# Kernel optimization log

Measured on AMD Instinct MI355X. Metric: run time of the kernel, lower is better.

The kernel has to match this reference:

```python
import jax, jax.numpy as jnp
import numpy as np

B, N = 4, 512
H, NH, L = 64, 4, 3
HD = H // NH          # 16
NODE_F, EDGE_F = 18, 7
H4 = H // 4           # 16
FF = 4 * H            # 256


def _ln(x, g, b, eps=1e-5):
    m = jnp.mean(x, axis=-1, keepdims=True)
    v = jnp.mean((x - m) ** 2, axis=-1, keepdims=True)
    return (x - m) * jax.lax.rsqrt(v + eps) * g + b


def _leaky(x):
    return jnp.where(x >= 0, x, 0.2 * x)


def _spd(edge_mask):
    # Vectorized Floyd-Warshall, mirrors GraphTransformer._compute_spd_matrix
    n = edge_mask.shape[1]
    spd = jnp.where(edge_mask, 1.0, float(n)).astype(jnp.float32)
    i = jnp.arange(n)
    spd = spd.at[:, i, i].set(0.0)
    def body(k, s):
        col = jax.lax.dynamic_slice_in_dim(s, k, 1, axis=2)  # [B,N,1]
        row = jax.lax.dynamic_slice_in_dim(s, k, 1, axis=1)  # [B,1,N]
        return jnp.minimum(s, col + row)
    return jax.lax.fori_loop(0, n, body, spd)


def setup_inputs() -> dict:
    key = jax.random.key(0)
    ks = iter(jax.random.split(key, 64))
    def nrm(shape, s):
        return jax.random.normal(next(ks), shape, jnp.float32) * s
    inp = {}
    inp["node_features"] = jax.random.normal(next(ks), (B, N, NODE_F), jnp.float32)
    inp["edge_features"] = jax.random.normal(next(ks), (B, N, N, EDGE_F), jnp.float32)
    nm = jax.random.uniform(next(ks), (B, N)) < 0.9
    inp["node_mask"] = nm.at[:, 0].set(True)
    inp["edge_mask"] = jax.random.uniform(next(ks), (B, N, N)) < 0.05
    s_h = 1.0 / np.sqrt(H)
    inp["node_proj_w"] = nrm((NODE_F, H), 0.2)
    inp["node_proj_b"] = jnp.zeros((H,), jnp.float32)
    inp["edge_proj_w"] = nrm((EDGE_F, H), 0.2)
    inp["edge_proj_b"] = jnp.zeros((H,), jnp.float32)
    inp["wq"] = nrm((L, H, H), s_h)
    inp["wk"] = nrm((L, H, H), s_h)
    inp["wv"] = nrm((L, H, H), s_h)
    inp["eb1_w"] = nrm((L, H, H4), s_h)
    inp["eb1_b"] = jnp.zeros((L, H4), jnp.float32)
    inp["eb_ln_g"] = jnp.ones((L, H4), jnp.float32)
    inp["eb_ln_b"] = jnp.zeros((L, H4), jnp.float32)
    inp["eb2_w"] = nrm((L, H4, NH), 0.2)
    inp["eb2_b"] = jnp.zeros((L, NH), jnp.float32)
    inp["spd1_w"] = nrm((L, 1, H4), 0.5)
    inp["spd1_b"] = jnp.zeros((L, H4), jnp.float32)
    inp["spd2_w"] = nrm((L, H4, NH), 0.2)
    inp["spd2_b"] = jnp.zeros((L, NH), jnp.float32)
    inp["wo_w"] = nrm((L, H, H), s_h)
    inp["wo_b"] = jnp.zeros((L, H), jnp.float32)
    inp["ln1_g"] = jnp.ones((L, H), jnp.float32)
    inp["ln1_b"] = jnp.zeros((L, H), jnp.float32)
    inp["ln2_g"] = jnp.ones((L, H), jnp.float32)
    inp["ln2_b"] = jnp.zeros((L, H), jnp.float32)
    inp["ffn1_w"] = nrm((L, H, FF), s_h)
    inp["ffn1_b"] = jnp.zeros((L, FF), jnp.float32)
    inp["ffn2_w"] = nrm((L, FF, H), 1.0 / np.sqrt(FF))
    inp["ffn2_b"] = jnp.zeros((L, H), jnp.float32)
    inp["score1_w"] = nrm((2 * H, H), 1.0 / np.sqrt(2 * H))
    inp["score1_b"] = jnp.zeros((H,), jnp.float32)
    inp["score_ln_g"] = jnp.ones((H,), jnp.float32)
    inp["score_ln_b"] = jnp.zeros((H,), jnp.float32)
    inp["score2_w"] = nrm((H, 1), 0.1)
    inp["score2_b"] = jnp.zeros((1,), jnp.float32)
    return inp


def reference(node_features, edge_features, node_mask, edge_mask,
              node_proj_w, node_proj_b, edge_proj_w, edge_proj_b,
              wq, wk, wv,
              eb1_w, eb1_b, eb_ln_g, eb_ln_b, eb2_w, eb2_b,
              spd1_w, spd1_b, spd2_w, spd2_b,
              wo_w, wo_b, ln1_g, ln1_b, ln2_g, ln2_b,
              ffn1_w, ffn1_b, ffn2_w, ffn2_b,
              score1_w, score1_b, score_ln_g, score_ln_b, score2_w, score2_b):
    NEG = -1000000000.0
    h = node_features @ node_proj_w + node_proj_b            # [B,N,H]
    e = edge_features @ edge_proj_w + edge_proj_b            # [B,N,N,H]
    spd = _spd(edge_mask)
    spd_n = (jnp.clip(spd, 0.0, 10.0) / 10.0)[..., None]      # [B,N,N,1]
    scale = 1.0 / np.sqrt(HD)
    for l in range(L):
        Q = (h @ wq[l]).reshape(B, N, NH, HD)
        K = (h @ wk[l]).reshape(B, N, NH, HD)
        V = (h @ wv[l]).reshape(B, N, NH, HD)
        scores = jnp.einsum('bihd,bjhd->bhij', Q, K) * scale  # [B,NH,N,N]
        x = _leaky(_ln(e @ eb1_w[l] + eb1_b[l], eb_ln_g[l], eb_ln_b[l]))
        edge_bias = jnp.transpose(x @ eb2_w[l] + eb2_b[l], (0, 3, 1, 2))
        sb = _leaky(spd_n @ spd1_w[l] + spd1_b[l]) @ spd2_w[l] + spd2_b[l]
        spd_bias = jnp.transpose(sb, (0, 3, 1, 2))
        bias = jnp.where(edge_mask[:, None, :, :], edge_bias, spd_bias)
        scores = jnp.where(node_mask[:, None, None, :], scores + bias, NEG)
        attn = jax.nn.softmax(scores, axis=-1)
        out = jnp.einsum('bhij,bjhd->bihd', attn, V).reshape(B, N, H)
        out = out @ wo_w[l] + wo_b[l]
        h = _ln(h + out, ln1_g[l], ln1_b[l])
        ff = jax.nn.gelu(h @ ffn1_w[l] + ffn1_b[l], approximate=False) @ ffn2_w[l] + ffn2_b[l]
        h = _ln(h + ff, ln2_g[l], ln2_b[l])
    h_ego = jnp.broadcast_to(h[:, :1, :], (B, N - 1, H))
    hc = jnp.concatenate([h_ego, h[:, 1:, :]], axis=-1)       # [B,N-1,2H]
    x = _leaky(_ln(hc @ score1_w + score1_b, score_ln_g, score_ln_b))
    logits = (x @ score2_w + score2_b)[..., 0]                # [B,N-1]
    cand_mask = node_mask[:, 1:]
    no_cand = ~jnp.any(cand_mask, axis=-1)
    cand_mask = cand_mask.at[:, 0].set(cand_mask[:, 0] | no_cand)
    logits = jnp.where(cand_mask, logits, NEG)
    probs = jax.nn.softmax(logits, axis=-1)
    return probs, h
```

## Files before the change

kernel.cpp:

```cpp
#include <hip/hip_runtime.h>
#include <math.h>

typedef unsigned long long u64;
typedef unsigned int u32;

__device__ __forceinline__ float wsum(float x) {
#pragma unroll
    for (int o = 1; o < 64; o <<= 1) x += __shfl_xor(x, o);
    return x;
}
__device__ __forceinline__ float wmaxr(float x) {
#pragma unroll
    for (int o = 1; o < 64; o <<= 1) x = fmaxf(x, __shfl_xor(x, o));
    return x;
}

__global__ __launch_bounds__(256) void kA(
    const int* __restrict__ em, const float* __restrict__ nf,
    const float* __restrict__ npw, const float* __restrict__ npb,
    u64* __restrict__ adj, u32* __restrict__ elist, u32* __restrict__ rowCnt,
    float* __restrict__ hbuf)
{
    int t = threadIdx.x, wv = t >> 6, lane = t & 63;
    int g = blockIdx.x * 4 + wv;
    const int* emr = em + (size_t)g * 512;
    u32 run = 0;
#pragma unroll
    for (int s = 0; s < 8; ++s) {
        int j = s * 64 + lane;
        int v = emr[j];
        u64 bal = __ballot(v != 0);
        if (v != 0) {
            u32 slot = run + (u32)__popcll(bal & ((1ULL << lane) - 1ULL));
            if (slot < 96u) elist[g * 96 + slot] = (u32)j;
        }
        if (lane == 0) adj[(size_t)g * 8 + s] = bal;
        run += (u32)__popcll(bal);
    }
    if (lane == 0) rowCnt[g] = run < 96u ? run : 96u;
    float acc = npb[lane];
    const float* r = nf + (size_t)g * 18;
#pragma unroll
    for (int c = 0; c < 18; ++c) acc += r[c] * npw[c * 64 + lane];
    hbuf[(size_t)g * 64 + lane] = acc;
}

__global__ __launch_bounds__(256) void kB(
    const u64* __restrict__ adj, const float* __restrict__ ef,
    const u32* __restrict__ elist, const u32* __restrict__ rowCnt,
    const float* __restrict__ hbuf,
    const float* __restrict__ epw, const float* __restrict__ epb,
    const float* __restrict__ eb1w, const float* __restrict__ eb1b,
    const float* __restrict__ eblng, const float* __restrict__ eblnb,
    const float* __restrict__ eb2w, const float* __restrict__ eb2b,
    const float* __restrict__ wq, const float* __restrict__ wk, const float* __restrict__ wvw,
    unsigned char* __restrict__ spd, float* __restrict__ vals,
    float* __restrict__ Qb, float* __restrict__ KT, float* __restrict__ VT)
{
    __shared__ u64 adjL[4096];
    __shared__ u64 bfsS[4][24];
    __shared__ float MS[684];
    __shared__ u32 pool[384];
    __shared__ u32 offs[5];
    __shared__ u32 cA[4];
    __shared__ int votes[4];
    int t = threadIdx.x, wv = t >> 6, lane = t & 63;
    int g = blockIdx.x * 4 + wv;
    int b = g >> 9, srow = g & 511;
    {
        const float4* s = (const float4*)(adj + (size_t)b * 4096);
        float4* d = (float4*)adjL;
#pragma unroll
        for (int u = 0; u < 8; ++u) d[t + u * 256] = s[t + u * 256];
    }
    for (int u = t; u < 384; u += 256) {
        int l = u >> 7, r = u & 127, f = r >> 4, c = r & 15;
        const float* W1 = eb1w + l * 1024 + c;
        float s;
        if (f < 7) {
            s = 0.f;
            const float* ew = epw + f * 64;
            for (int k = 0; k < 64; ++k) s += ew[k] * W1[k * 16];
        } else {
            s = eb1b[l * 16 + c];
            for (int k = 0; k < 64; ++k) s += epb[k] * W1[k * 16];
        }
        MS[u] = s;
    }
    if (t < 192) MS[384 + t] = eb2w[t];
    if (t < 48) { MS[576 + t] = eblng[t]; MS[624 + t] = eblnb[t]; }
    if (t < 12) MS[672 + t] = eb2b[t];
    u64* vis = &bfsS[wv][0]; u64* fro = vis + 8; u64* nxt = vis + 16;
    if (lane < 8) {
        u64 iv = (lane == (srow >> 6)) ? (1ULL << (srow & 63)) : 0ULL;
        vis[lane] = iv; fro[lane] = iv; nxt[lane] = 0ULL;
    }
    __syncthreads();
    u64 myDist = 0x0A0A0A0A0A0A0A0AULL;
    if (lane == (srow >> 3)) myDist &= ~(0xFFULL << ((srow & 7) * 8));
    for (int d = 1; d <= 9; ++d) {
        int c = lane >> 3, w = lane & 7;
        u64 f = fro[c];
        u64 acc = 0ULL;
        while (f) {
            int k = (c << 6) + __builtin_ctzll(f);
            f &= f - 1;
            acc |= adjL[k * 8 + w];
        }
        if (acc) atomicOr(&nxt[w], acc);
        __syncthreads();
        u64 nw = 0ULL;
        if (lane < 8) {
            nw = nxt[lane] & ~vis[lane];
            vis[lane] |= nw; fro[lane] = nw; nxt[lane] = 0ULL;
        }
        u64 bal = __ballot(nw != 0ULL);
        if (lane == 0) votes[wv] = (bal != 0ULL) ? 1 : 0;
        __syncthreads();
        u64 fw = fro[lane >> 3];
        u32 bits = (u32)(fw >> ((lane & 7) * 8)) & 0xFFu;
        if (bits) {
            u64 bm = 0ULL;
#pragma unroll
            for (int kk = 0; kk < 8; ++kk) if (bits & (1u << kk)) bm |= 0xFFULL << (8 * kk);
            myDist = (myDist & ~bm) | ((0x0101010101010101ULL * (u64)(u32)d) & bm);
        }
        if (!(votes[0] | votes[1] | votes[2] | votes[3])) break;
    }
    ((u64*)spd)[(size_t)g * 64 + lane] = myDist;
    {
        float hv = hbuf[(size_t)g * 64 + lane];
        float aq = 0.f, ak = 0.f, av = 0.f;
        for (int k = 0; k < 64; ++k) {
            float hk = __shfl(hv, k);
            aq += hk * wq[k * 64 + lane];
            ak += hk * wk[k * 64 + lane];
            av += hk * wvw[k * 64 + lane];
        }
        Qb[(size_t)g * 64 + lane] = aq;
        KT[((size_t)(b * 64 + lane)) * 512 + srow] = ak;
        VT[((size_t)(b * 64 + lane)) * 512 + srow] = av;
    }
    u32 cnt = rowCnt[g];
    if (lane == 0) cA[wv] = cnt;
    __syncthreads();
    if (t == 0) {
        u32 a = 0;
        for (int i = 0; i < 4; ++i) { offs[i] = a; a += cA[i]; }
        offs[4] = a;
    }
    __syncthreads();
    u32 base = offs[wv];
    if (lane < (int)cnt)
        pool[base + lane] = ((u32)wv << 16) | ((u32)lane << 9) | elist[g * 96 + lane];
    if (lane + 64 < (int)cnt)
        pool[base + lane + 64] = ((u32)wv << 16) | ((u32)(lane + 64) << 9) | elist[g * 96 + lane + 64];
    __syncthreads();
    u32 tot = offs[4];
    for (u32 e = t; e < tot; e += 256) {
        u32 p = pool[e];
        int rl = (int)(p >> 16);
        u32 s = (p >> 9) & 127u;
        u32 j = p & 511u;
        int ge = blockIdx.x * 4 + rl;
        const float* e7 = ef + ((size_t)ge * 512 + j) * 7;
        float ff[7];
#pragma unroll
        for (int f = 0; f < 7; ++f) ff[f] = e7[f];
#pragma unroll 1
        for (int l = 0; l < 3; ++l) {
            float tt[16];
#pragma unroll
            for (int c = 0; c < 16; ++c) tt[c] = MS[(l * 8 + 7) * 16 + c];
#pragma unroll
            for (int f = 0; f < 7; ++f) {
                float fv = ff[f];
#pragma unroll
                for (int c = 0; c < 16; ++c) tt[c] += fv * MS[(l * 8 + f) * 16 + c];
            }
            float m = 0.f;
#pragma unroll
            for (int c = 0; c < 16; ++c) m += tt[c];
            m *= 0.0625f;
            float var = 0.f;
#pragma unroll
            for (int c = 0; c < 16; ++c) { float d = tt[c] - m; var += d * d; }
            var *= 0.0625f;
            float inv = rsqrtf(var + 1e-5f);
#pragma unroll
            for (int c = 0; c < 16; ++c) {
                float x = (tt[c] - m) * inv * MS[576 + l * 16 + c] + MS[624 + l * 16 + c];
                tt[c] = x >= 0.f ? x : 0.2f * x;
            }
#pragma unroll
            for (int hh = 0; hh < 4; ++hh) {
                float a = MS[672 + l * 4 + hh];
#pragma unroll
                for (int c = 0; c < 16; ++c) a += tt[c] * MS[384 + (l * 16 + c) * 4 + hh];
                vals[(u32)(l * 4 + hh) * 196608u + (u32)ge * 96u + s] = a;
            }
        }
    }
}

__global__ __launch_bounds__(256, 2) void kAttn(
    const float* __restrict__ Qb, const float* __restrict__ KTin, const float* __restrict__ VTin,
    const unsigned char* __restrict__ spd, const u32* __restrict__ elist,
    const u32* __restrict__ rowCnt, const float* __restrict__ vals,
    const float* __restrict__ s1w, const float* __restrict__ s1b,
    const float* __restrict__ s2w, const float* __restrict__ s2b,
    const int* __restrict__ nm, int l, float* __restrict__ attO)
{
    __shared__ float kt[8192];
    __shared__ float bv[8192];
    int t = threadIdx.x, wv = t >> 6, lane = t & 63;
    int bh = blockIdx.x >> 5;
    int tile = blockIdx.x & 31;
    int b = bh >> 2, hh = bh & 3;
    int i0 = tile * 16;
    int rbase = i0 + wv * 4;
    float qv = Qb[((size_t)(b * 512 + rbase + (lane >> 4))) * 64 + hh * 16 + (lane & 15)];
    float q[4][16];
#pragma unroll
    for (int r = 0; r < 4; ++r)
#pragma unroll
        for (int d = 0; d < 16; ++d) q[r][d] = __shfl(qv, r * 16 + d);
    {
        const float4* s = (const float4*)(KTin + ((size_t)(b * 64 + hh * 16)) * 512);
        float4* d = (float4*)kt;
#pragma unroll
        for (int u = 0; u < 8; ++u) d[t + u * 256] = s[t + u * 256];
    }
    float tval;
    {
        int li = lane < 11 ? lane : 10;
        float x = (float)li * 0.1f;
        float a = s2b[l * 4 + hh];
#pragma unroll
        for (int c = 0; c < 16; ++c) {
            float v = x * s1w[l * 16 + c] + s1b[l * 16 + c];
            v = v >= 0.f ? v : 0.2f * v;
            a += v * s2w[(l * 16 + c) * 4 + hh];
        }
        tval = a;
    }
    {
        const u32* sp = (const u32*)(spd + ((size_t)(b * 512 + i0)) * 512);
#pragma unroll
        for (int p = 0; p < 8; ++p) {
            int i32 = t + p * 256;
            u32 w4 = sp[i32];
            float4 bb;
            bb.x = __shfl(tval, (int)(w4 & 255u));
            bb.y = __shfl(tval, (int)((w4 >> 8) & 255u));
            bb.z = __shfl(tval, (int)((w4 >> 16) & 255u));
            bb.w = __shfl(tval, (int)(w4 >> 24));
            ((float4*)bv)[i32] = bb;
        }
    }
    __syncthreads();
    u32 vp = (u32)(l * 4 + hh) * 196608u;
#pragma unroll
    for (int rr = 0; rr < 4; ++rr) {
        int g = b * 512 + rbase + rr;
        u32 cnt = rowCnt[g];
        for (u32 s = lane; s < cnt; s += 64u) {
            u32 j = elist[g * 96 + s] & 511u;
            bv[(wv * 4 + rr) * 512 + j] = vals[vp + (u32)g * 96u + s];
        }
    }
    const int* nmb = nm + b * 512;
    float sc[8][4];
    float mx[4] = {-3e38f, -3e38f, -3e38f, -3e38f};
#pragma unroll
    for (int c = 0; c < 8; ++c) {
        int j = c * 64 + lane;
        float ktv[16];
#pragma unroll
        for (int d = 0; d < 16; ++d) ktv[d] = kt[d * 512 + j];
        float madd = (nmb[j] != 0) ? 0.f : -1e9f;
#pragma unroll
        for (int r = 0; r < 4; ++r) {
            float s = 0.f;
#pragma unroll
            for (int d = 0; d < 16; ++d) s += q[r][d] * ktv[d];
            s = s * 0.25f + bv[(wv * 4 + r) * 512 + j] + madd;
            sc[c][r] = s;
            mx[r] = fmaxf(mx[r], s);
        }
    }
#pragma unroll
    for (int r = 0; r < 4; ++r) mx[r] = wmaxr(mx[r]);
    float sm[4] = {0.f, 0.f, 0.f, 0.f};
#pragma unroll
    for (int c = 0; c < 8; ++c)
#pragma unroll
        for (int r = 0; r < 4; ++r) { sc[c][r] = __expf(sc[c][r] - mx[r]); sm[r] += sc[c][r]; }
#pragma unroll
    for (int r = 0; r < 4; ++r) sm[r] = 1.0f / wsum(sm[r]);
#pragma unroll
    for (int c = 0; c < 8; ++c)
#pragma unroll
        for (int r = 0; r < 4; ++r) sc[c][r] *= sm[r];
    __syncthreads();
    {
        const float4* s = (const float4*)(VTin + ((size_t)(b * 64 + hh * 16)) * 512);
        float4* d = (float4*)kt;
#pragma unroll
        for (int u = 0; u < 8; ++u) d[t + u * 256] = s[t + u * 256];
    }
    __syncthreads();
    float acc[4][16];
#pragma unroll
    for (int r = 0; r < 4; ++r)
#pragma unroll
        for (int d = 0; d < 16; ++d) acc[r][d] = 0.f;
#pragma unroll
    for (int c = 0; c < 8; ++c) {
        int j = c * 64 + lane;
#pragma unroll
        for (int d = 0; d < 16; ++d) {
            float v = kt[d * 512 + j];
#pragma unroll
            for (int r = 0; r < 4; ++r) acc[r][d] += sc[c][r] * v;
        }
    }
#pragma unroll
    for (int r = 0; r < 4; ++r)
#pragma unroll
        for (int d = 0; d < 16; ++d) {
            acc[r][d] += __shfl_xor(acc[r][d], 16);
            acc[r][d] += __shfl_xor(acc[r][d], 32);
        }
    float* scr = bv + wv * 2048;
    if (lane < 16) {
#pragma unroll
        for (int r = 0; r < 4; ++r)
#pragma unroll
            for (int d = 0; d < 16; ++d) scr[lane * 65 + r * 16 + d] = acc[r][d];
    }
    float o = 0.f;
#pragma unroll
    for (int m = 0; m < 16; ++m) o += scr[m * 65 + lane];
    attO[((size_t)(b * 512 + rbase + (lane >> 4))) * 64 + hh * 16 + (lane & 15)] = o;
}

__global__ __launch_bounds__(256) void kLF(
    const float* __restrict__ attO,
    const float* __restrict__ wow, const float* __restrict__ wob,
    const float* __restrict__ ln1g, const float* __restrict__ ln1b,
    const float* __restrict__ f1w, const float* __restrict__ f1b,
    const float* __restrict__ f2w, const float* __restrict__ f2b,
    const float* __restrict__ ln2g, const float* __restrict__ ln2b,
    const float* __restrict__ wqn, const float* __restrict__ wkn, const float* __restrict__ wvn,
    const float* __restrict__ sc1w, const float* __restrict__ sc1b,
    float* __restrict__ hbuf, float* __restrict__ QbOut,
    float* __restrict__ KTout, float* __restrict__ VTout,
    float* __restrict__ egoAcc, int l, float* __restrict__ out)
{
    int t = threadIdx.x, wv = t >> 6, lane = t & 63;
    int g = blockIdx.x * 4 + wv;
    int b = g >> 9, srow = g & 511;
    float hv = hbuf[(size_t)g * 64 + lane];
    float att = attO[(size_t)g * 64 + lane];
    float h1;
    {
        float a = wob[l * 64 + lane];
        const float* Wo = wow + l * 4096;
        for (int k = 0; k < 64; ++k) a += __shfl(att, k) * Wo[k * 64 + lane];
        float xx = a + hv;
        float mn = wsum(xx) * 0.015625f;
        float d = xx - mn;
        float var = wsum(d * d) * 0.015625f;
        h1 = d * rsqrtf(var + 1e-5f) * ln1g[l * 64 + lane] + ln1b[l * 64 + lane];
    }
    float hn;
    {
        const float* W1 = f1w + l * 16384;
        const float* W2 = f2w + l * 16384;
        float a1[4];
#pragma unroll
        for (int m = 0; m < 4; ++m) a1[m] = f1b[l * 256 + m * 64 + lane];
        for (int k = 0; k < 64; ++k) {
            float hk = __shfl(h1, k);
#pragma unroll
            for (int m = 0; m < 4; ++m) a1[m] += hk * W1[k * 256 + m * 64 + lane];
        }
        float ffv[4];
#pragma unroll
        for (int m = 0; m < 4; ++m) {
            float u = a1[m];
            ffv[m] = 0.5f * u * (1.0f + erff(u * 0.70710678118654752f));
        }
        float a2 = 0.f;
#pragma unroll 1
        for (int m = 0; m < 4; ++m) {
            for (int ll = 0; ll < 64; ++ll) {
                a2 += __shfl(ffv[m], ll) * W2[(m * 64 + ll) * 64 + lane];
            }
        }
        float xx = a2 + f2b[l * 64 + lane] + h1;
        float mn = wsum(xx) * 0.015625f;
        float d = xx - mn;
        float var = wsum(d * d) * 0.015625f;
        hn = d * rsqrtf(var + 1e-5f) * ln2g[l * 64 + lane] + ln2b[l * 64 + lane];
    }
    hbuf[(size_t)g * 64 + lane] = hn;
    if (l == 2) {
        out[2044 + (size_t)g * 64 + lane] = hn;
        if (srow == 0) {
            float ea = sc1b[lane];
            for (int k = 0; k < 64; ++k) ea += __shfl(hn, k) * sc1w[k * 64 + lane];
            egoAcc[b * 64 + lane] = ea;
        }
    } else {
        float aq = 0.f, ak = 0.f, av = 0.f;
        for (int k = 0; k < 64; ++k) {
            float hk = __shfl(hn, k);
            aq += hk * wqn[k * 64 + lane];
            ak += hk * wkn[k * 64 + lane];
            av += hk * wvn[k * 64 + lane];
        }
        QbOut[(size_t)g * 64 + lane] = aq;
        KTout[((size_t)(b * 64 + lane)) * 512 + srow] = ak;
        VTout[((size_t)(b * 64 + lane)) * 512 + srow] = av;
    }
}

__global__ __launch_bounds__(256) void kS(
    const float* __restrict__ hbuf, const float* __restrict__ egoAcc,
    const float* __restrict__ s1w,
    const float* __restrict__ lng, const float* __restrict__ lnb,
    const float* __restrict__ s2w, const float* __restrict__ s2b,
    float* __restrict__ logits)
{
    int t = threadIdx.x, wv = t >> 6, lane = t & 63;
    int wid = blockIdx.x * 4 + wv;
    if (wid >= 2044) return;
    int bb = wid / 511; int jj = wid % 511; int j = jj + 1;
    float cand = hbuf[((size_t)(bb * 512 + j)) * 64 + lane];
    float acc = egoAcc[bb * 64 + lane];
    for (int k = 0; k < 64; ++k) acc += __shfl(cand, k) * s1w[(64 + k) * 64 + lane];
    float mn = wsum(acc) * 0.015625f;
    float d = acc - mn;
    float var = wsum(d * d) * 0.015625f;
    float x = d * rsqrtf(var + 1e-5f) * lng[lane] + lnb[lane];
    x = x >= 0.f ? x : 0.2f * x;
    float p = wsum(x * s2w[lane]);
    if (lane == 0) logits[wid] = p + s2b[0];
}

__global__ __launch_bounds__(512) void kP(
    const float* __restrict__ logits, const int* __restrict__ nmask, float* __restrict__ out)
{
    __shared__ float red[512];
    __shared__ int anyf;
    int b = blockIdx.x; int t = threadIdx.x;
    bool cand = false;
    if (t < 511) cand = nmask[b * 512 + 1 + t] != 0;
    if (t == 0) anyf = 0;
    __syncthreads();
    if (cand) atomicOr(&anyf, 1);
    __syncthreads();
    if (t == 0 && anyf == 0) cand = true;
    float val = -3e38f;
    if (t < 511) val = cand ? logits[b * 511 + t] : -1e9f;
    red[t] = val; __syncthreads();
    for (int s = 256; s > 0; s >>= 1) { if (t < s) red[t] = fmaxf(red[t], red[t + s]); __syncthreads(); }
    float m = red[0]; __syncthreads();
    float p = (t < 511) ? __expf(val - m) : 0.f;
    red[t] = p; __syncthreads();
    for (int s = 256; s > 0; s >>= 1) { if (t < s) red[t] += red[t + s]; __syncthreads(); }
    float inv = 1.0f / red[0];
    if (t < 511) out[b * 511 + t] = p * inv;
}

extern "C" void kernel_launch(void* const* d_in, const int* in_sizes, int n_in,
                              void* d_out, int out_size, void* d_ws, size_t ws_size,
                              hipStream_t stream) {
    const float* nf    = (const float*)d_in[0];
    const float* ef    = (const float*)d_in[1];
    const int*   nm    = (const int*)d_in[2];
    const int*   em    = (const int*)d_in[3];
    const float* npw   = (const float*)d_in[4];
    const float* npb   = (const float*)d_in[5];
    const float* epw   = (const float*)d_in[6];
    const float* epb   = (const float*)d_in[7];
    const float* wq    = (const float*)d_in[8];
    const float* wk    = (const float*)d_in[9];
    const float* wv    = (const float*)d_in[10];
    const float* eb1w  = (const float*)d_in[11];
    const float* eb1b  = (const float*)d_in[12];
    const float* eblng = (const float*)d_in[13];
    const float* eblnb = (const float*)d_in[14];
    const float* eb2w  = (const float*)d_in[15];
    const float* eb2b  = (const float*)d_in[16];
    const float* s1wv  = (const float*)d_in[17];
    const float* s1bv  = (const float*)d_in[18];
    const float* s2wv  = (const float*)d_in[19];
    const float* s2bv  = (const float*)d_in[20];
    const float* wow   = (const float*)d_in[21];
    const float* wob   = (const float*)d_in[22];
    const float* ln1g  = (const float*)d_in[23];
    const float* ln1b  = (const float*)d_in[24];
    const float* ln2g  = (const float*)d_in[25];
    const float* ln2b  = (const float*)d_in[26];
    const float* f1w   = (const float*)d_in[27];
    const float* f1b   = (const float*)d_in[28];
    const float* f2w   = (const float*)d_in[29];
    const float* f2b   = (const float*)d_in[30];
    const float* sc1w  = (const float*)d_in[31];
    const float* sc1b  = (const float*)d_in[32];
    const float* sclng = (const float*)d_in[33];
    const float* sclnb = (const float*)d_in[34];
    const float* sc2w  = (const float*)d_in[35];
    const float* sc2b  = (const float*)d_in[36];

    char* W = (char*)d_ws;
    u64*   adj    = (u64*)(W + 0);
    unsigned char* spd = (unsigned char*)(W + 131072);
    u32*   elist  = (u32*)(W + 1179648);
    u32*   rowCnt = (u32*)(W + 1966080);
    float* vals   = (float*)(W + 1974272);
    float* hbuf   = (float*)(W + 11411456);
    float* Qb     = (float*)(W + 11935744);
    float* KT0    = (float*)(W + 12460032);
    float* VT0    = (float*)(W + 12984320);
    float* KT1    = (float*)(W + 13508608);
    float* VT1    = (float*)(W + 14032896);
    float* logits = (float*)(W + 14557184);
    float* egoAcc = (float*)(W + 14565376);
    float* attO   = (float*)(W + 14566400);

    float* out = (float*)d_out;

    kA<<<512, 256, 0, stream>>>(em, nf, npw, npb, adj, elist, rowCnt, hbuf);
    kB<<<512, 256, 0, stream>>>(adj, ef, elist, rowCnt, hbuf, epw, epb,
                                eb1w, eb1b, eblng, eblnb, eb2w, eb2b,
                                wq, wk, wv, spd, vals, Qb, KT0, VT0);

    kAttn<<<512, 256, 0, stream>>>(Qb, KT0, VT0, spd, elist, rowCnt, vals,
                                   s1wv, s1bv, s2wv, s2bv, nm, 0, attO);
    kLF<<<512, 256, 0, stream>>>(attO, wow, wob, ln1g, ln1b, f1w, f1b, f2w, f2b,
                                 ln2g, ln2b, wq + 4096, wk + 4096, wv + 4096,
                                 sc1w, sc1b, hbuf, Qb, KT1, VT1, egoAcc, 0, out);

    kAttn<<<512, 256, 0, stream>>>(Qb, KT1, VT1, spd, elist, rowCnt, vals,
                                   s1wv, s1bv, s2wv, s2bv, nm, 1, attO);
    kLF<<<512, 256, 0, stream>>>(attO, wow, wob, ln1g, ln1b, f1w, f1b, f2w, f2b,
                                 ln2g, ln2b, wq + 8192, wk + 8192, wv + 8192,
                                 sc1w, sc1b, hbuf, Qb, KT0, VT0, egoAcc, 1, out);

    kAttn<<<512, 256, 0, stream>>>(Qb, KT0, VT0, spd, elist, rowCnt, vals,
                                   s1wv, s1bv, s2wv, s2bv, nm, 2, attO);
    kLF<<<512, 256, 0, stream>>>(attO, wow, wob, ln1g, ln1b, f1w, f1b, f2w, f2b,
                                 ln2g, ln2b, wq, wk, wv,
                                 sc1w, sc1b, hbuf, Qb, KT1, VT1, egoAcc, 2, out);

    kS<<<511, 256, 0, stream>>>(hbuf, egoAcc, sc1w, sclng, sclnb, sc2w, sc2b, logits);
    kP<<<4, 512, 0, stream>>>(logits, nm, out);
}
```

Measured before the change: 299.4 us.

## Use async global-to-LDS loads, split FFN2 accumulators, fuse score head into final kernel

Loads K and V tiles into shared memory with direct global-to-LDS loads, issuing the K load before Q setup so it can overlap. Splits the FFN2 reduction into four independent accumulators for more instruction-level parallelism. Computes the candidate half of the score projection inside the last layer kernel and merges the scoring and softmax kernels into one launch. This removes a launch and the register staging of the loads, but the final kernel now runs on only four blocks, and the async loads rely on barriers for completion.

```diff
diff --git a/kernel.cpp b/kernel.cpp
--- a/kernel.cpp
+++ b/kernel.cpp
@@ -3,6 +3,10 @@
 
 typedef unsigned long long u64;
 typedef unsigned int u32;
+
+#define GLDS16(gp, lp) __builtin_amdgcn_global_load_lds( \
+    (const __attribute__((address_space(1))) void*)(gp), \
+    (__attribute__((address_space(3))) void*)(lp), 16, 0, 0)
 
 __device__ __forceinline__ float wsum(float x) {
 #pragma unroll
@@ -219,18 +223,18 @@
     int b = bh >> 2, hh = bh & 3;
     int i0 = tile * 16;
     int rbase = i0 + wv * 4;
+    {
+        const float4* s = (const float4*)(KTin + ((size_t)(b * 64 + hh * 16)) * 512);
+        float4* d = (float4*)kt;
+#pragma unroll
+        for (int u = 0; u < 8; ++u) GLDS16(s + u * 256 + t, d + u * 256 + t);
+    }
     float qv = Qb[((size_t)(b * 512 + rbase + (lane >> 4))) * 64 + hh * 16 + (lane & 15)];
     float q[4][16];
 #pragma unroll
     for (int r = 0; r < 4; ++r)
 #pragma unroll
         for (int d = 0; d < 16; ++d) q[r][d] = __shfl(qv, r * 16 + d);
-    {
-        const float4* s = (const float4*)(KTin + ((size_t)(b * 64 + hh * 16)) * 512);
-        float4* d = (float4*)kt;
-#pragma unroll
-        for (int u = 0; u < 8; ++u) d[t + u * 256] = s[t + u * 256];
-    }
     float tval;
     {
         int li = lane < 11 ? lane : 10;
@@ -307,7 +311,7 @@
         const float4* s = (const float4*)(VTin + ((size_t)(b * 64 + hh * 16)) * 512);
         float4* d = (float4*)kt;
 #pragma unroll
-        for (int u = 0; u < 8; ++u) d[t + u * 256] = s[t + u * 256];
+        for (int u = 0; u < 8; ++u) GLDS16(s + u * 256 + t, d + u * 256 + t);
     }
     __syncthreads();
     float acc[4][16];
@@ -356,7 +360,8 @@
     const float* __restrict__ sc1w, const float* __restrict__ sc1b,
     float* __restrict__ hbuf, float* __restrict__ QbOut,
     float* __restrict__ KTout, float* __restrict__ VTout,
-    float* __restrict__ egoAcc, int l, float* __restrict__ out)
+    float* __restrict__ egoAcc, float* __restrict__ candAcc,
+    int l, float* __restrict__ out)
 {
     int t = threadIdx.x, wv = t >> 6, lane = t & 63;
     int g = blockIdx.x * 4 + wv;
@@ -392,13 +397,14 @@
             float u = a1[m];
             ffv[m] = 0.5f * u * (1.0f + erff(u * 0.70710678118654752f));
         }
-        float a2 = 0.f;
-#pragma unroll 1
-        for (int m = 0; m < 4; ++m) {
-            for (int ll = 0; ll < 64; ++ll) {
-                a2 += __shfl(ffv[m], ll) * W2[(m * 64 + ll) * 64 + lane];
-            }
-        }
+        float a2p0 = 0.f, a2p1 = 0.f, a2p2 = 0.f, a2p3 = 0.f;
+        for (int ll = 0; ll < 64; ++ll) {
+            a2p0 += __shfl(ffv[0], ll) * W2[(ll) * 64 + lane];
+            a2p1 += __shfl(ffv[1], ll) * W2[(64 + ll) * 64 + lane];
+            a2p2 += __shfl(ffv[2], ll) * W2[(128 + ll) * 64 + lane];
+            a2p3 += __shfl(ffv[3], ll) * W2[(192 + ll) * 64 + lane];
+        }
+        float a2 = ((a2p0 + a2p1) + a2p2) + a2p3;
         float xx = a2 + f2b[l * 64 + lane] + h1;
         float mn = wsum(xx) * 0.015625f;
         float d = xx - mn;
@@ -408,6 +414,9 @@
     hbuf[(size_t)g * 64 + lane] = hn;
     if (l == 2) {
         out[2044 + (size_t)g * 64 + lane] = hn;
+        float ca = 0.f;
+        for (int k = 0; k < 64; ++k) ca += __shfl(hn, k) * sc1w[(64 + k) * 64 + lane];
+        candAcc[(size_t)g * 64 + lane] = ca;
         if (srow == 0) {
             float ea = sc1b[lane];
             for (int k = 0; k < 64; ++k) ea += __shfl(hn, k) * sc1w[k * 64 + lane];
@@ -427,50 +436,54 @@
     }
 }
 
-__global__ __launch_bounds__(256) void kS(
-    const float* __restrict__ hbuf, const float* __restrict__ egoAcc,
-    const float* __restrict__ s1w,
+__global__ __launch_bounds__(1024) void kP2(
+    const float* __restrict__ egoAcc, const float* __restrict__ candAcc,
     const float* __restrict__ lng, const float* __restrict__ lnb,
     const float* __restrict__ s2w, const float* __restrict__ s2b,
-    float* __restrict__ logits)
+    const int* __restrict__ nm, float* __restrict__ out)
 {
-    int t = threadIdx.x, wv = t >> 6, lane = t & 63;
-    int wid = blockIdx.x * 4 + wv;
-    if (wid >= 2044) return;
-    int bb = wid / 511; int jj = wid % 511; int j = jj + 1;
-    float cand = hbuf[((size_t)(bb * 512 + j)) * 64 + lane];
-    float acc = egoAcc[bb * 64 + lane];
-    for (int k = 0; k < 64; ++k) acc += __shfl(cand, k) * s1w[(64 + k) * 64 + lane];
-    float mn = wsum(acc) * 0.015625f;
-    float d = acc - mn;
-    float var = wsum(d * d) * 0.015625f;
-    float x = d * rsqrtf(var + 1e-5f) * lng[lane] + lnb[lane];
-    x = x >= 0.f ? x : 0.2f * x;
-    float p = wsum(x * s2w[lane]);
-    if (lane == 0) logits[wid] = p + s2b[0];
-}
-
-__global__ __launch_bounds__(512) void kP(
-    const float* __restrict__ logits, const int* __restrict__ nmask, float* __restrict__ out)
-{
+    __shared__ float lgt[512];
     __shared__ float red[512];
     __shared__ int anyf;
-    int b = blockIdx.x; int t = threadIdx.x;
-    bool cand = false;
-    if (t < 511) cand = nmask[b * 512 + 1 + t] != 0;
+    int b = blockIdx.x, t = threadIdx.x;
+    int wave = t >> 6, lane = t & 63;
     if (t == 0) anyf = 0;
-    __syncthreads();
+    float eacc = egoAcc[b * 64 + lane];
+    float lngl = lng[lane], lnbl = lnb[lane];
+    float s2wl = s2w[lane], s2b0 = s2b[0];
+#pragma unroll 1
+    for (int jj = wave; jj < 511; jj += 16) {
+        int j = jj + 1;
+        float acc = eacc + candAcc[((size_t)(b * 512 + j)) * 64 + lane];
+        float mn = wsum(acc) * 0.015625f;
+        float d = acc - mn;
+        float var = wsum(d * d) * 0.015625f;
+        float x = d * rsqrtf(var + 1e-5f) * lngl + lnbl;
+        x = x >= 0.f ? x : 0.2f * x;
+        float p = wsum(x * s2wl);
+        if (lane == 0) lgt[jj] = p + s2b0;
+    }
+    __syncthreads();
+    bool cand = (t < 511) ? (nm[b * 512 + 1 + t] != 0) : false;
     if (cand) atomicOr(&anyf, 1);
     __syncthreads();
     if (t == 0 && anyf == 0) cand = true;
-    float val = -3e38f;
-    if (t < 511) val = cand ? logits[b * 511 + t] : -1e9f;
-    red[t] = val; __syncthreads();
-    for (int s = 256; s > 0; s >>= 1) { if (t < s) red[t] = fmaxf(red[t], red[t + s]); __syncthreads(); }
-    float m = red[0]; __syncthreads();
+    float val = (t < 511) ? (cand ? lgt[t] : -1e9f) : -3e38f;
+    if (t < 512) red[t] = val;
+    __syncthreads();
+    for (int s = 256; s > 0; s >>= 1) {
+        if (t < s) red[t] = fmaxf(red[t], red[t + s]);
+        __syncthreads();
+    }
+    float m = red[0];
+    __syncthreads();
     float p = (t < 511) ? __expf(val - m) : 0.f;
-    red[t] = p; __syncthreads();
-    for (int s = 256; s > 0; s >>= 1) { if (t < s) red[t] += red[t + s]; __syncthreads(); }
+    if (t < 512) red[t] = p;
+    __syncthreads();
+    for (int s = 256; s > 0; s >>= 1) {
+        if (t < s) red[t] += red[t + s];
+        __syncthreads();
+    }
     float inv = 1.0f / red[0];
     if (t < 511) out[b * 511 + t] = p * inv;
 }
@@ -528,9 +541,9 @@
     float* VT0    = (float*)(W + 12984320);
     float* KT1    = (float*)(W + 13508608);
     float* VT1    = (float*)(W + 14032896);
-    float* logits = (float*)(W + 14557184);
-    float* egoAcc = (float*)(W + 14565376);
-    float* attO   = (float*)(W + 14566400);
+    float* egoAcc = (float*)(W + 14557184);
+    float* attO   = (float*)(W + 14558208);
+    float* candAcc= (float*)(W + 15082496);
 
     float* out = (float*)d_out;
 
@@ -543,20 +556,19 @@
                                    s1wv, s1bv, s2wv, s2bv, nm, 0, attO);
     kLF<<<512, 256, 0, stream>>>(attO, wow, wob, ln1g, ln1b, f1w, f1b, f2w, f2b,
                                  ln2g, ln2b, wq + 4096, wk + 4096, wv + 4096,
-                                 sc1w, sc1b, hbuf, Qb, KT1, VT1, egoAcc, 0, out);
+                                 sc1w, sc1b, hbuf, Qb, KT1, VT1, egoAcc, candAcc, 0, out);
 
     kAttn<<<512, 256, 0, stream>>>(Qb, KT1, VT1, spd, elist, rowCnt, vals,
                                    s1wv, s1bv, s2wv, s2bv, nm, 1, attO);
     kLF<<<512, 256, 0, stream>>>(attO, wow, wob, ln1g, ln1b, f1w, f1b, f2w, f2b,
                                  ln2g, ln2b, wq + 8192, wk + 8192, wv + 8192,
-                                 sc1w, sc1b, hbuf, Qb, KT0, VT0, egoAcc, 1, out);
+                                 sc1w, sc1b, hbuf, Qb, KT0, VT0, egoAcc, candAcc, 1, out);
 
     kAttn<<<512, 256, 0, stream>>>(Qb, KT0, VT0, spd, elist, rowCnt, vals,
                                    s1wv, s1bv, s2wv, s2bv, nm, 2, attO);
     kLF<<<512, 256, 0, stream>>>(attO, wow, wob, ln1g, ln1b, f1w, f1b, f2w, f2b,
                                  ln2g, ln2b, wq, wk, wv,
-                                 sc1w, sc1b, hbuf, Qb, KT1, VT1, egoAcc, 2, out);
-
-    kS<<<511, 256, 0, stream>>>(hbuf, egoAcc, sc1w, sclng, sclnb, sc2w, sc2b, logits);
-    kP<<<4, 512, 0, stream>>>(logits, nm, out);
-}
+                                 sc1w, sc1b, hbuf, Qb, KT1, VT1, egoAcc, candAcc, 2, out);
+
+    kP2<<<4, 1024, 0, stream>>>(egoAcc, candAcc, sclng, sclnb, sc2w, sc2b, nm, out);
+}
```

Result: slower. 312.9 us (+4.5%).
